# Performance work log

Hardware: AMD Instinct MI355X
Metric: run time of the kernel (lower is better)

## Reference

```python
import jax, jax.numpy as jnp
import numpy as np

BLOCK = 16
N1, N2, RANK = 64, 64, 64
# E2M1 (NVFP4) representable magnitudes
_FP4_GRID = jnp.array([0.0, 0.5, 1.0, 1.5, 2.0, 3.0, 4.0, 6.0], dtype=jnp.float32)
_FP4_MIDS = (_FP4_GRID[1:] + _FP4_GRID[:-1]) / 2.0


def quantize_to_nvfp4(x, block_size=BLOCK):
    """Per-block (last dim, block_size=16) NVFP4 fake-quant: amax scale to 6.0, round to E2M1 grid, dequant."""
    shape = x.shape
    xb = x.reshape(shape[:-1] + (shape[-1] // block_size, block_size))
    amax = jnp.max(jnp.abs(xb), axis=-1, keepdims=True)
    scale = jnp.maximum(amax / 6.0, 1e-8)
    y = xb / scale
    idx = jnp.searchsorted(_FP4_MIDS, jnp.abs(y), side='right')  # nearest grid index
    q = _FP4_GRID[idx] * jnp.sign(y)
    return (q * scale).reshape(shape)


def setup_inputs() -> dict:
    key = jax.random.key(0)
    ks = jax.random.split(key, 6)
    B, S, n, m, r = 4, 2048, 4096, 4096, RANK
    return {
        'x': jax.random.normal(ks[0], (B, S, n), dtype=jnp.float32),
        'smooth_scale': jax.random.uniform(ks[1], (n,), dtype=jnp.float32, minval=0.2, maxval=2.0),
        'a_q': jax.random.normal(ks[2], (m, r), dtype=jnp.float32) * 0.05,
        'b_q': jax.random.normal(ks[3], (N1, r), dtype=jnp.float32) * 0.1,
        'c_q_t': jax.random.normal(ks[4], (r, N2), dtype=jnp.float32) * 0.1,
        'bias': jax.random.normal(ks[5], (m,), dtype=jnp.float32),
    }


def reference(x, smooth_scale, a_q, b_q, c_q_t, bias):
    # smooth + activation quant
    x_q = quantize_to_nvfp4(x * smooth_scale, BLOCK)
    # reshape (..., n) -> (..., n1, n2)
    x_3d = x_q.reshape(x.shape[:-1] + (N1, N2))
    # contract C: F.linear(x_3d, c_q_t) -> (..., n1, r)
    h1 = jnp.einsum('bsij,rj->bsir', x_3d, c_q_t)
    # contract B: (h1 * B).sum over n1 -> (..., r)
    h2 = jnp.einsum('bsir,ir->bsr', h1, b_q)
    # contract A: h2 @ A.T + bias -> (..., m)
    out = jnp.einsum('bsr,mr->bsm', h2, a_q) + bias
    return out
```

## Files before the change

### kernel.cpp

```cpp
#include <hip/hip_runtime.h>

typedef float f32x4 __attribute__((ext_vector_type(4)));
typedef short s16x8 __attribute__((ext_vector_type(8)));
typedef short s16x4 __attribute__((ext_vector_type(4)));
typedef unsigned short u16;

#define N_COLS 4096
#define RANK 64

__device__ __forceinline__ unsigned f_asuint(float f) { union { float f; unsigned u; } v; v.f = f; return v.u; }
__device__ __forceinline__ float f_asfloat(unsigned u) { union { unsigned u; float f; } v; v.u = u; return v.f; }
__device__ __forceinline__ short f2bf(float f) {
  unsigned u = f_asuint(f);
  return (short)((u + 0x7fffu + ((u >> 16) & 1u)) >> 16);
}

__device__ __forceinline__ void gload_lds16(const void* g, void* l) {
  __builtin_amdgcn_global_load_lds(
      (const __attribute__((address_space(1))) unsigned int*)g,
      (__attribute__((address_space(3))) unsigned int*)l,
      16, 0, 0);
}

__global__ __launch_bounds__(256) void k_prep(const float* __restrict__ b_q,
                                              const float* __restrict__ c_q_t,
                                              const float* __restrict__ a_q,
                                              u16* __restrict__ W,
                                              u16* __restrict__ a_bf) {
  int j = blockIdx.x * 256 + threadIdx.x;
  if (j < 32768) {
    int r = j >> 9;
    int n0 = (j << 3) & 4095;
    float b = b_q[(n0 >> 6) * RANK + r];
    const f32x4* cp = reinterpret_cast<const f32x4*>(c_q_t + (r << 6) + (n0 & 63));
    f32x4 c0 = cp[0], c1 = cp[1];
    s16x8 w;
    w[0] = f2bf(b * c0.x); w[1] = f2bf(b * c0.y); w[2] = f2bf(b * c0.z); w[3] = f2bf(b * c0.w);
    w[4] = f2bf(b * c1.x); w[5] = f2bf(b * c1.y); w[6] = f2bf(b * c1.z); w[7] = f2bf(b * c1.w);
    *reinterpret_cast<s16x8*>(W + ((size_t)j << 3)) = w;
  } else {
    int j2 = j - 32768;
    const f32x4* ap = reinterpret_cast<const f32x4*>(a_q + ((size_t)j2 << 3));
    f32x4 a0 = ap[0], a1 = ap[1];
    s16x8 v;
    v[0] = f2bf(a0.x); v[1] = f2bf(a0.y); v[2] = f2bf(a0.z); v[3] = f2bf(a0.w);
    v[4] = f2bf(a1.x); v[5] = f2bf(a1.y); v[6] = f2bf(a1.z); v[7] = f2bf(a1.w);
    *reinterpret_cast<s16x8*>(a_bf + ((size_t)j2 << 3)) = v;
  }
}

__global__ __launch_bounds__(256, 4) void k_h2(const float* __restrict__ x,
                                               const float* __restrict__ smooth,
                                               const u16* __restrict__ W,
                                               float* __restrict__ h2p,
                                               int T) {
  const int t0 = blockIdx.x * 16;
  const int kb = blockIdx.y;
  const int wave = threadIdx.x >> 6;
  const int lane = threadIdx.x & 63;
  const int quad = lane >> 4;
  const int tl = lane & 15;
  const int K0b = kb << 10;

  __shared__ float xbuf[2][4096];
  __shared__ float sml[1024];

  gload_lds16(smooth + K0b + wave * 256 + (lane << 2), &sml[wave * 256]);

  const int colL = lane << 2;
#pragma unroll
  for (int q = 0; q < 4; ++q) {
    int tok = q * 4 + wave;
    int c = colL ^ ((tok & 7) << 2);
    gload_lds16(x + (size_t)(t0 + tok) * N_COLS + K0b + c, &xbuf[0][tok * 256]);
  }
  __syncthreads();

  f32x4 acc0 = {0.f, 0.f, 0.f, 0.f};
  f32x4 acc1 = {0.f, 0.f, 0.f, 0.f};
  f32x4 acc2 = {0.f, 0.f, 0.f, 0.f};
  f32x4 acc3 = {0.f, 0.f, 0.f, 0.f};

  const int c0w = wave * 64 + quad * 8;
  const int swz = (tl & 7) << 2;
  const u16* wpB = W + (size_t)tl * N_COLS + K0b + c0w;

#pragma unroll
  for (int t = 0; t < 4; ++t) {
    if (t + 1 < 4) {
#pragma unroll
      for (int q = 0; q < 4; ++q) {
        int tok = q * 4 + wave;
        int c = colL ^ ((tok & 7) << 2);
        gload_lds16(x + (size_t)(t0 + tok) * N_COLS + K0b + (t + 1) * 256 + c,
                    &xbuf[(t + 1) & 1][tok * 256]);
      }
    }

    s16x8 w8[2][4];
#pragma unroll
    for (int si = 0; si < 2; ++si)
#pragma unroll
      for (int i = 0; i < 4; ++i)
        w8[si][i] = *reinterpret_cast<const s16x8*>(
            wpB + t * 256 + si * 32 + (size_t)i * 16 * N_COLS);

    const float* xb = xbuf[t & 1];
#pragma unroll
    for (int si = 0; si < 2; ++si) {
      const int cs = c0w + si * 32;
      f32x4 xa = *reinterpret_cast<const f32x4*>(xb + tl * 256 + (cs ^ swz));
      f32x4 xv = *reinterpret_cast<const f32x4*>(xb + tl * 256 + ((cs + 4) ^ swz));
      f32x4 sa = *reinterpret_cast<const f32x4*>(sml + t * 256 + cs);
      f32x4 sb = *reinterpret_cast<const f32x4*>(sml + t * 256 + cs + 4);

      float xs[8];
      xs[0] = xa.x * sa.x; xs[1] = xa.y * sa.y; xs[2] = xa.z * sa.z; xs[3] = xa.w * sa.w;
      xs[4] = xv.x * sb.x; xs[5] = xv.y * sb.y; xs[6] = xv.z * sb.z; xs[7] = xv.w * sb.w;

      float amax = fabsf(xs[0]);
#pragma unroll
      for (int j = 1; j < 8; ++j) amax = fmaxf(amax, fabsf(xs[j]));
      amax = fmaxf(amax, __shfl_xor(amax, 16));
      float scale = fmaxf(amax * (1.0f / 6.0f), 1e-8f);

      const float th0 = 0.25f * scale, th1 = 0.75f * scale, th2 = 1.25f * scale,
                  th3 = 1.75f * scale, th4 = 2.5f * scale, th5 = 3.5f * scale,
                  th6 = 5.0f * scale;
      s16x8 af;
#pragma unroll
      for (int j = 0; j < 8; ++j) {
        float ax = fabsf(xs[j]);
        float q = (ax >= th0) ? 0.5f : 0.0f;
        q = (ax >= th1) ? 1.0f : q;
        q = (ax >= th2) ? 1.5f : q;
        q = (ax >= th3) ? 2.0f : q;
        q = (ax >= th4) ? 3.0f : q;
        q = (ax >= th5) ? 4.0f : q;
        q = (ax >= th6) ? 6.0f : q;
        float xq = q * scale;
        xq = f_asfloat(f_asuint(xq) | (f_asuint(xs[j]) & 0x80000000u));
        af[j] = f2bf(xq);
      }

      acc0 = __builtin_amdgcn_mfma_f32_16x16x32_bf16(af, w8[si][0], acc0, 0, 0, 0);
      acc1 = __builtin_amdgcn_mfma_f32_16x16x32_bf16(af, w8[si][1], acc1, 0, 0, 0);
      acc2 = __builtin_amdgcn_mfma_f32_16x16x32_bf16(af, w8[si][2], acc2, 0, 0, 0);
      acc3 = __builtin_amdgcn_mfma_f32_16x16x32_bf16(af, w8[si][3], acc3, 0, 0, 0);
    }
    __syncthreads();
  }

  float* red = &xbuf[0][0];
  float* rw = red + wave * 1024 + (quad * 4) * 64 + tl;
#pragma unroll
  for (int reg = 0; reg < 4; ++reg) {
    rw[reg * 64 + 0]  = acc0[reg];
    rw[reg * 64 + 16] = acc1[reg];
    rw[reg * 64 + 32] = acc2[reg];
    rw[reg * 64 + 48] = acc3[reg];
  }
  __syncthreads();
  {
    const f32x4* r4 = reinterpret_cast<const f32x4*>(red);
    f32x4 v = r4[threadIdx.x];
#pragma unroll
    for (int p = 1; p < 4; ++p) {
      f32x4 u = r4[p * 256 + threadIdx.x];
      v.x += u.x; v.y += u.y; v.z += u.z; v.w += u.w;
    }
    int t = threadIdx.x >> 4;
    int rr = (threadIdx.x & 15) * 4;
    *reinterpret_cast<f32x4*>(h2p + ((size_t)kb * T + t0 + t) * RANK + rr) = v;
  }
}

__global__ __launch_bounds__(256, 4) void k_gemm2(const float* __restrict__ h2p,
                                                  const u16* __restrict__ a_bf,
                                                  const float* __restrict__ bias,
                                                  float* __restrict__ out,
                                                  int T) {
  const int t0 = blockIdx.y * 32;
  const int m0 = blockIdx.x * 256;
  const int wave = threadIdx.x >> 6;
  const int lane = threadIdx.x & 63;
  const int quad = lane >> 4;
  const int tl = lane & 15;

  __shared__ u16 h2l[32 * 72];
  __shared__ float tile[16 * 260];

  {
    int t = threadIdx.x >> 3;
    int r0 = (threadIdx.x & 7) * 8;
    const float* p = h2p + (size_t)(t0 + t) * RANK + r0;
    f32x4 v0 = *reinterpret_cast<const f32x4*>(p);
    f32x4 v1 = *reinterpret_cast<const f32x4*>(p + 4);
#pragma unroll
    for (int kb = 1; kb < 4; ++kb) {
      const float* q = p + (size_t)kb * T * RANK;
      f32x4 u0 = *reinterpret_cast<const f32x4*>(q);
      f32x4 u1 = *reinterpret_cast<const f32x4*>(q + 4);
      v0.x += u0.x; v0.y += u0.y; v0.z += u0.z; v0.w += u0.w;
      v1.x += u1.x; v1.y += u1.y; v1.z += u1.z; v1.w += u1.w;
    }
    s16x8 h;
    h[0] = f2bf(v0.x); h[1] = f2bf(v0.y); h[2] = f2bf(v0.z); h[3] = f2bf(v0.w);
    h[4] = f2bf(v1.x); h[5] = f2bf(v1.y); h[6] = f2bf(v1.z); h[7] = f2bf(v1.w);
    *reinterpret_cast<s16x8*>(h2l + t * 72 + r0) = h;
  }
  __syncthreads();

  const u16* hp0 = h2l + tl * 72 + quad * 8;
  const u16* hp1 = hp0 + 16 * 72;
  const u16* ap = a_bf + (size_t)(m0 + wave * 64 + tl) * RANK + quad * 8;

  f32x4 acc[2][4] = {};

#pragma unroll
  for (int o = 0; o < 64; o += 32) {
    s16x8 a0 = *reinterpret_cast<const s16x8*>(hp0 + o);
    s16x8 a1 = *reinterpret_cast<const s16x8*>(hp1 + o);
#pragma unroll
    for (int mg = 0; mg < 4; ++mg) {
      s16x8 bfr = *reinterpret_cast<const s16x8*>(ap + (size_t)mg * 16 * RANK + o);
      acc[0][mg] = __builtin_amdgcn_mfma_f32_16x16x32_bf16(a0, bfr, acc[0][mg], 0, 0, 0);
      acc[1][mg] = __builtin_amdgcn_mfma_f32_16x16x32_bf16(a1, bfr, acc[1][mg], 0, 0, 0);
    }
  }

#pragma unroll
  for (int tg = 0; tg < 2; ++tg) {
    if (tg) __syncthreads();
#pragma unroll
    for (int mg = 0; mg < 4; ++mg)
#pragma unroll
      for (int reg = 0; reg < 4; ++reg)
        tile[(quad * 4 + reg) * 260 + wave * 64 + mg * 16 + tl] = acc[tg][mg][reg];
    __syncthreads();
#pragma unroll
    for (int i = 0; i < 4; ++i) {
      int idx = threadIdx.x + i * 256;
      int row = idx >> 6;
      int c4 = (idx & 63) << 2;
      f32x4 v = *reinterpret_cast<const f32x4*>(tile + row * 260 + c4);
      f32x4 b = *reinterpret_cast<const f32x4*>(bias + m0 + c4);
      f32x4 ov;
      ov.x = v.x + b.x; ov.y = v.y + b.y; ov.z = v.z + b.z; ov.w = v.w + b.w;
      __builtin_nontemporal_store(ov,
        reinterpret_cast<f32x4*>(out + (size_t)(t0 + tg * 16 + row) * N_COLS + m0 + c4));
    }
  }
}

extern "C" void kernel_launch(void* const* d_in, const int* in_sizes, int n_in,
                              void* d_out, int out_size, void* d_ws, size_t ws_size,
                              hipStream_t stream) {
  const float* x      = (const float*)d_in[0];
  const float* smooth = (const float*)d_in[1];
  const float* a_q    = (const float*)d_in[2];
  const float* b_q    = (const float*)d_in[3];
  const float* c_q_t  = (const float*)d_in[4];
  const float* bias   = (const float*)d_in[5];
  float* out = (float*)d_out;

  const int T = in_sizes[0] / N_COLS;

  u16* W     = (u16*)d_ws;
  u16* a_bf  = (u16*)((char*)d_ws + 524288);
  float* h2p = (float*)((char*)d_ws + 1048576);

  k_prep<<<256, 256, 0, stream>>>(b_q, c_q_t, a_q, W, a_bf);
  dim3 gh(T / 16, 4);
  k_h2<<<gh, 256, 0, stream>>>(x, smooth, W, h2p, T);
  dim3 g2(N_COLS / 256, T / 32);
  k_gemm2<<<g2, 256, 0, stream>>>(h2p, a_bf, bias, out, T);
}
```

Baseline: 268.9 us.

## Enlarge gemm2 token tile to 64, convert A to bf16 in-register, drop nontemporal stores

```diff
diff --git a/kernel.cpp b/kernel.cpp
--- a/kernel.cpp
+++ b/kernel.cpp
@@ -24,29 +24,17 @@
 
 __global__ __launch_bounds__(256) void k_prep(const float* __restrict__ b_q,
                                               const float* __restrict__ c_q_t,
-                                              const float* __restrict__ a_q,
-                                              u16* __restrict__ W,
-                                              u16* __restrict__ a_bf) {
+                                              u16* __restrict__ W) {
   int j = blockIdx.x * 256 + threadIdx.x;
-  if (j < 32768) {
-    int r = j >> 9;
-    int n0 = (j << 3) & 4095;
-    float b = b_q[(n0 >> 6) * RANK + r];
-    const f32x4* cp = reinterpret_cast<const f32x4*>(c_q_t + (r << 6) + (n0 & 63));
-    f32x4 c0 = cp[0], c1 = cp[1];
-    s16x8 w;
-    w[0] = f2bf(b * c0.x); w[1] = f2bf(b * c0.y); w[2] = f2bf(b * c0.z); w[3] = f2bf(b * c0.w);
-    w[4] = f2bf(b * c1.x); w[5] = f2bf(b * c1.y); w[6] = f2bf(b * c1.z); w[7] = f2bf(b * c1.w);
-    *reinterpret_cast<s16x8*>(W + ((size_t)j << 3)) = w;
-  } else {
-    int j2 = j - 32768;
-    const f32x4* ap = reinterpret_cast<const f32x4*>(a_q + ((size_t)j2 << 3));
-    f32x4 a0 = ap[0], a1 = ap[1];
-    s16x8 v;
-    v[0] = f2bf(a0.x); v[1] = f2bf(a0.y); v[2] = f2bf(a0.z); v[3] = f2bf(a0.w);
-    v[4] = f2bf(a1.x); v[5] = f2bf(a1.y); v[6] = f2bf(a1.z); v[7] = f2bf(a1.w);
-    *reinterpret_cast<s16x8*>(a_bf + ((size_t)j2 << 3)) = v;
-  }
+  int r = j >> 9;
+  int n0 = (j << 3) & 4095;
+  float b = b_q[(n0 >> 6) * RANK + r];
+  const f32x4* cp = reinterpret_cast<const f32x4*>(c_q_t + (r << 6) + (n0 & 63));
+  f32x4 c0 = cp[0], c1 = cp[1];
+  s16x8 w;
+  w[0] = f2bf(b * c0.x); w[1] = f2bf(b * c0.y); w[2] = f2bf(b * c0.z); w[3] = f2bf(b * c0.w);
+  w[4] = f2bf(b * c1.x); w[5] = f2bf(b * c1.y); w[6] = f2bf(b * c1.z); w[7] = f2bf(b * c1.w);
+  *reinterpret_cast<s16x8*>(W + ((size_t)j << 3)) = w;
 }
 
 __global__ __launch_bounds__(256, 4) void k_h2(const float* __restrict__ x,
@@ -176,62 +164,79 @@
 }
 
 __global__ __launch_bounds__(256, 4) void k_gemm2(const float* __restrict__ h2p,
-                                                  const u16* __restrict__ a_bf,
+                                                  const float* __restrict__ a_q,
                                                   const float* __restrict__ bias,
                                                   float* __restrict__ out,
                                                   int T) {
-  const int t0 = blockIdx.y * 32;
+  const int t0 = blockIdx.y * 64;
   const int m0 = blockIdx.x * 256;
   const int wave = threadIdx.x >> 6;
   const int lane = threadIdx.x & 63;
   const int quad = lane >> 4;
   const int tl = lane & 15;
 
-  __shared__ u16 h2l[32 * 72];
+  __shared__ u16 h2l[64 * 72];
   __shared__ float tile[16 * 260];
 
   {
-    int t = threadIdx.x >> 3;
-    int r0 = (threadIdx.x & 7) * 8;
+    int t = threadIdx.x >> 2;
+    int r0 = (threadIdx.x & 3) * 16;
     const float* p = h2p + (size_t)(t0 + t) * RANK + r0;
     f32x4 v0 = *reinterpret_cast<const f32x4*>(p);
     f32x4 v1 = *reinterpret_cast<const f32x4*>(p + 4);
+    f32x4 v2 = *reinterpret_cast<const f32x4*>(p + 8);
+    f32x4 v3 = *reinterpret_cast<const f32x4*>(p + 12);
 #pragma unroll
     for (int kb = 1; kb < 4; ++kb) {
       const float* q = p + (size_t)kb * T * RANK;
       f32x4 u0 = *reinterpret_cast<const f32x4*>(q);
       f32x4 u1 = *reinterpret_cast<const f32x4*>(q + 4);
+      f32x4 u2 = *reinterpret_cast<const f32x4*>(q + 8);
+      f32x4 u3 = *reinterpret_cast<const f32x4*>(q + 12);
       v0.x += u0.x; v0.y += u0.y; v0.z += u0.z; v0.w += u0.w;
       v1.x += u1.x; v1.y += u1.y; v1.z += u1.z; v1.w += u1.w;
-    }
-    s16x8 h;
-    h[0] = f2bf(v0.x); h[1] = f2bf(v0.y); h[2] = f2bf(v0.z); h[3] = f2bf(v0.w);
-    h[4] = f2bf(v1.x); h[5] = f2bf(v1.y); h[6] = f2bf(v1.z); h[7] = f2bf(v1.w);
-    *reinterpret_cast<s16x8*>(h2l + t * 72 + r0) = h;
+      v2.x += u2.x; v2.y += u2.y; v2.z += u2.z; v2.w += u2.w;
+      v3.x += u3.x; v3.y += u3.y; v3.z += u3.z; v3.w += u3.w;
+    }
+    s16x8 h0, h1;
+    h0[0] = f2bf(v0.x); h0[1] = f2bf(v0.y); h0[2] = f2bf(v0.z); h0[3] = f2bf(v0.w);
+    h0[4] = f2bf(v1.x); h0[5] = f2bf(v1.y); h0[6] = f2bf(v1.z); h0[7] = f2bf(v1.w);
+    h1[0] = f2bf(v2.x); h1[1] = f2bf(v2.y); h1[2] = f2bf(v2.z); h1[3] = f2bf(v2.w);
+    h1[4] = f2bf(v3.x); h1[5] = f2bf(v3.y); h1[6] = f2bf(v3.z); h1[7] = f2bf(v3.w);
+    *reinterpret_cast<s16x8*>(h2l + t * 72 + r0) = h0;
+    *reinterpret_cast<s16x8*>(h2l + t * 72 + r0 + 8) = h1;
   }
   __syncthreads();
 
-  const u16* hp0 = h2l + tl * 72 + quad * 8;
-  const u16* hp1 = hp0 + 16 * 72;
-  const u16* ap = a_bf + (size_t)(m0 + wave * 64 + tl) * RANK + quad * 8;
-
-  f32x4 acc[2][4] = {};
+  const float* aq = a_q + (size_t)(m0 + wave * 64 + tl) * RANK + quad * 8;
+
+  f32x4 acc[4][4] = {};
 
 #pragma unroll
   for (int o = 0; o < 64; o += 32) {
-    s16x8 a0 = *reinterpret_cast<const s16x8*>(hp0 + o);
-    s16x8 a1 = *reinterpret_cast<const s16x8*>(hp1 + o);
+    s16x8 afr[4];
 #pragma unroll
     for (int mg = 0; mg < 4; ++mg) {
-      s16x8 bfr = *reinterpret_cast<const s16x8*>(ap + (size_t)mg * 16 * RANK + o);
-      acc[0][mg] = __builtin_amdgcn_mfma_f32_16x16x32_bf16(a0, bfr, acc[0][mg], 0, 0, 0);
-      acc[1][mg] = __builtin_amdgcn_mfma_f32_16x16x32_bf16(a1, bfr, acc[1][mg], 0, 0, 0);
-    }
-  }
-
-#pragma unroll
-  for (int tg = 0; tg < 2; ++tg) {
-    if (tg) __syncthreads();
+      const float* aq2 = aq + (size_t)mg * 16 * RANK + o;
+      f32x4 a0 = *reinterpret_cast<const f32x4*>(aq2);
+      f32x4 a1 = *reinterpret_cast<const f32x4*>(aq2 + 4);
+      afr[mg][0] = f2bf(a0.x); afr[mg][1] = f2bf(a0.y);
+      afr[mg][2] = f2bf(a0.z); afr[mg][3] = f2bf(a0.w);
+      afr[mg][4] = f2bf(a1.x); afr[mg][5] = f2bf(a1.y);
+      afr[mg][6] = f2bf(a1.z); afr[mg][7] = f2bf(a1.w);
+    }
+#pragma unroll
+    for (int tg = 0; tg < 4; ++tg) {
+      s16x8 hfr = *reinterpret_cast<const s16x8*>(h2l + (tg * 16 + tl) * 72 + quad * 8 + o);
+#pragma unroll
+      for (int mg = 0; mg < 4; ++mg)
+        acc[tg][mg] = __builtin_amdgcn_mfma_f32_16x16x32_bf16(hfr, afr[mg], acc[tg][mg], 0, 0, 0);
+    }
+  }
+
+#pragma unroll
+  for (int tg = 0; tg < 4; ++tg) {
+    __syncthreads();
 #pragma unroll
     for (int mg = 0; mg < 4; ++mg)
 #pragma unroll
@@ -247,8 +252,7 @@
       f32x4 b = *reinterpret_cast<const f32x4*>(bias + m0 + c4);
       f32x4 ov;
       ov.x = v.x + b.x; ov.y = v.y + b.y; ov.z = v.z + b.z; ov.w = v.w + b.w;
-      __builtin_nontemporal_store(ov,
-        reinterpret_cast<f32x4*>(out + (size_t)(t0 + tg * 16 + row) * N_COLS + m0 + c4));
+      *reinterpret_cast<f32x4*>(out + (size_t)(t0 + tg * 16 + row) * N_COLS + m0 + c4) = ov;
     }
   }
 }
@@ -267,12 +271,11 @@
   const int T = in_sizes[0] / N_COLS;
 
   u16* W     = (u16*)d_ws;
-  u16* a_bf  = (u16*)((char*)d_ws + 524288);
-  float* h2p = (float*)((char*)d_ws + 1048576);
-
-  k_prep<<<256, 256, 0, stream>>>(b_q, c_q_t, a_q, W, a_bf);
+  float* h2p = (float*)((char*)d_ws + 524288);
+
+  k_prep<<<128, 256, 0, stream>>>(b_q, c_q_t, W);
   dim3 gh(T / 16, 4);
   k_h2<<<gh, 256, 0, stream>>>(x, smooth, W, h2p, T);
-  dim3 g2(N_COLS / 256, T / 32);
-  k_gemm2<<<g2, 256, 0, stream>>>(h2p, a_bf, bias, out, T);
-}
+  dim3 g2(N_COLS / 256, T / 64);
+  k_gemm2<<<g2, 256, 0, stream>>>(h2p, a_q, bias, out, T);
+}
```

Measured after the change: 277.9 us. 3.4% more time.
